# Kernel optimization log

Hardware: AMD Instinct MI355X
Metric: run time of the kernel (lower is better)

The kernel has to match this reference:

```python
import jax, jax.numpy as jnp
import numpy as np

HEADS = 8

def setup_inputs() -> dict:
    key = jax.random.key(0)
    ks = jax.random.split(key, 7)
    B, N, M, C = 4, 2048, 2048, 512
    s = 0.02
    return {
        "hidden_states": jax.random.normal(ks[0], (B, N, C), jnp.float32),
        "encoder_states": jax.random.normal(ks[1], (B, M, C), jnp.float32),
        "Wq": jax.random.normal(ks[2], (C, C), jnp.float32) * s,
        "Wk": jax.random.normal(ks[3], (C, C), jnp.float32) * s,
        "Wv": jax.random.normal(ks[4], (C, C), jnp.float32) * s,
        "Wo": jax.random.normal(ks[5], (C, C), jnp.float32) * s,
        "bo": jnp.zeros((C,), jnp.float32),
    }

def reference(hidden_states, encoder_states, Wq, Wk, Wv, Wo, bo):
    B, N, C = hidden_states.shape
    M = encoder_states.shape[1]
    H = HEADS
    dh = C // H
    scale = dh ** -0.5  # q.shape[-1] ** -0.5 in FlashAttentionFunction / attn.scale
    # projections (to_q/to_k/to_v, no bias as in diffusers CrossAttention)
    q = (hidden_states @ Wq).reshape(B, N, H, dh).transpose(0, 2, 1, 3)   # [B,H,N,dh]
    k = (encoder_states @ Wk).reshape(B, M, H, dh).transpose(0, 2, 1, 3)  # [B,H,M,dh]
    v = (encoder_states @ Wv).reshape(B, M, H, dh).transpose(0, 2, 1, 3)  # [B,H,M,dh]
    # baddbmm(scores) -> softmax -> bmm(values); no mask, non-causal
    scores = jnp.einsum('bhnd,bhmd->bhnm', q, k) * scale                  # [B,H,N,M]
    probs = jax.nn.softmax(scores, axis=-1)
    out = jnp.einsum('bhnm,bhmd->bhnd', probs, v)                         # [B,H,N,dh]
    out = out.transpose(0, 2, 1, 3).reshape(B, N, C)                      # batch_to_head_dim
    return out @ Wo + bo                                                  # to_out[0]; to_out[1] is dropout (identity at eval)
```

## Files before the change

kernel.cpp:

```cpp
#include <hip/hip_runtime.h>
#include <stdint.h>
#include <stddef.h>

typedef __bf16 bf16x8 __attribute__((ext_vector_type(8)));
typedef float f32x4 __attribute__((ext_vector_type(4)));
typedef float f32x16 __attribute__((ext_vector_type(16)));
typedef int int4v __attribute__((ext_vector_type(4)));
typedef unsigned short u16;
typedef unsigned int u32;

__device__ __forceinline__ u16 f2bf(float f) {
    union { float f; unsigned u; } x; x.f = f;
    unsigned r = x.u + 0x7fffu + ((x.u >> 16) & 1u);
    return (u16)(r >> 16);
}

__device__ __forceinline__ float fexp2(float x) { return __builtin_amdgcn_exp2f(x); }

__device__ __forceinline__ u32 cvtpk(float lo, float hi) {
    u32 r;
    asm("v_cvt_pk_bf16_f32 %0, %1, %2" : "=v"(r) : "v"(lo), "v"(hi));
    return r;
}

__device__ __forceinline__ void perm32swap(u32& a, u32& b) {
    asm("v_permlane32_swap_b32 %0, %1" : "+v"(a), "+v"(b));
}

__device__ __forceinline__ f32x16 mfma32(bf16x8 a, bf16x8 b, f32x16 c) {
    return __builtin_amdgcn_mfma_f32_32x32x16_bf16(a, b, c, 0, 0, 0);
}

__device__ __forceinline__ void gl16(const void* g, void* l) {
    __builtin_amdgcn_global_load_lds(
        (const __attribute__((address_space(1))) void*)g,
        (__attribute__((address_space(3))) void*)l, 16, 0, 0);
}

__global__ __launch_bounds__(256) void wtrans4(
        const float* __restrict__ Wq, const float* __restrict__ Wk,
        const float* __restrict__ Wv, const float* __restrict__ Wo,
        u16* __restrict__ oq, u16* __restrict__ ok,
        u16* __restrict__ ov, u16* __restrict__ oo) {
    const int z = blockIdx.z;
    const float* W = (z == 0) ? Wq : (z == 1) ? Wk : (z == 2) ? Wv : Wo;
    u16* O = (z == 0) ? oq : (z == 1) ? ok : (z == 2) ? ov : oo;
    int t  = blockIdx.x * 256 + threadIdx.x;
    int g  = t >> 12;
    int k0 = (t >> 9) & 7;
    int n  = t & 511;
    float v[8];
#pragma unroll
    for (int j = 0; j < 8; ++j)
        v[j] = W[(size_t)(k0 * 64 + g * 8 + j) * 512 + n];
    int gs = g ^ (n & 7);
    u16* dst = O + ((size_t)(k0 * 512 + n) * 8 + gs) * 8;
    ushort4 a, b;
    a.x = f2bf(v[0]); a.y = f2bf(v[1]); a.z = f2bf(v[2]); a.w = f2bf(v[3]);
    b.x = f2bf(v[4]); b.y = f2bf(v[5]); b.z = f2bf(v[6]); b.w = f2bf(v[7]);
    *(ushort4*)dst = a;
    *(ushort4*)(dst + 4) = b;
}

__global__ __launch_bounds__(256) void gemm_qkv(
        const float* __restrict__ hidden, const float* __restrict__ enc,
        const u16* __restrict__ wq, const u16* __restrict__ wk, const u16* __restrict__ wv,
        u16* __restrict__ qo, u16* __restrict__ ko, u16* __restrict__ vo) {
    __shared__ __align__(16) u16 As[128 * 64];
    __shared__ __align__(16) u16 Bs[128 * 64];
    const int z = blockIdx.z;
    const float* A = (z == 0) ? hidden : enc;
    const u16* Bp = (z == 0) ? wq : (z == 1) ? wk : wv;
    const int tid = threadIdx.x, lane = tid & 63, wave = tid >> 6;
    const int wr = (wave >> 1) * 64, wc = (wave & 1) * 64;
    const int brow = blockIdx.x * 128, bcol = blockIdx.y * 128;
    const int lrow = lane & 15;
    const int sr = tid >> 3, sc = tid & 7;

    f32x4 acc[4][4] = {};

    for (int k0s = 0; k0s < 8; ++k0s) {
        const u16* bsrc = Bp + ((size_t)(k0s * 512 + bcol) * 64) + (size_t)(wave * 256 + lane) * 8;
#pragma unroll
        for (int i = 0; i < 4; ++i)
            gl16(bsrc + i * 512, (char*)Bs + wave * 4096 + i * 1024);
#pragma unroll
        for (int i = 0; i < 4; ++i) {
            int r = i * 32 + sr;
            const float* src = A + (size_t)(brow + r) * 512 + k0s * 64 + sc * 8;
            float4 f0 = *(const float4*)src, f1 = *(const float4*)(src + 4);
            int4v w;
            w[0] = cvtpk(f0.x, f0.y); w[1] = cvtpk(f0.z, f0.w);
            w[2] = cvtpk(f1.x, f1.y); w[3] = cvtpk(f1.z, f1.w);
            *(int4v*)((char*)As + r * 128 + ((sc ^ (r & 7)) << 4)) = w;
        }
        __syncthreads();
#pragma unroll
        for (int kc = 0; kc < 2; ++kc) {
            const int kg = kc * 4 + (lane >> 4);
            bf16x8 af[4], bfr[4];
#pragma unroll
            for (int m = 0; m < 4; ++m) {
                int r = wr + m * 16 + lrow;
                af[m] = *(const bf16x8*)((char*)As + r * 128 + ((kg ^ (r & 7)) << 4));
            }
#pragma unroll
            for (int n = 0; n < 4; ++n) {
                int r = wc + n * 16 + lrow;
                bfr[n] = *(const bf16x8*)((char*)Bs + r * 128 + ((kg ^ (r & 7)) << 4));
            }
#pragma unroll
            for (int m = 0; m < 4; ++m)
#pragma unroll
                for (int n = 0; n < 4; ++n)
                    acc[m][n] = __builtin_amdgcn_mfma_f32_16x16x32_bf16(af[m], bfr[n], acc[m][n], 0, 0, 0);
        }
        __syncthreads();
    }

#pragma unroll
    for (int m = 0; m < 4; ++m) {
        int gr0 = brow + wr + m * 16 + ((lane >> 4) << 2);
#pragma unroll
        for (int n = 0; n < 4; ++n) {
            int gc = bcol + wc + n * 16 + lrow;
            int hh = gc >> 6, d = gc & 63;
            int b = gr0 >> 11;
            int bh2 = b * 8 + hh;
            if (z == 0) {
                int nn = gr0 & 2047;
#pragma unroll
                for (int j = 0; j < 4; ++j)
                    qo[((size_t)bh2 * 2048 + nn + j) * 64 + d] =
                        f2bf(acc[m][n][j] * (0.125f * 1.44269504f));
            } else if (z == 1) {
                int kc2 = d >> 4, hl2 = (d >> 3) & 1, e = d & 7;
#pragma unroll
                for (int j = 0; j < 4; ++j) {
                    int nn = (gr0 & 2047) + j;
                    size_t off = (((size_t)bh2 * 64 + (nn >> 5)) * 4 + kc2) * 512
                               + (size_t)((nn & 31) + 32 * hl2) * 8 + e;
                    ko[off] = f2bf(acc[m][n][j]);
                }
            } else {
                int nn0 = gr0 & 2047;
                int slice = ((nn0 >> 4) & 1) * 2 + (d >> 5);
                int lanev = (d & 31) + 32 * ((nn0 >> 3) & 1);
                size_t off = (((size_t)bh2 * 64 + (nn0 >> 5)) * 4 + slice) * 512
                           + (size_t)lanev * 8 + (nn0 & 7);
                ushort4 pk;
                pk.x = f2bf(acc[m][n][0]); pk.y = f2bf(acc[m][n][1]);
                pk.z = f2bf(acc[m][n][2]); pk.w = f2bf(acc[m][n][3]);
                *(ushort4*)(vo + off) = pk;
            }
        }
    }
}

__global__ __launch_bounds__(256) void gemm_out(
        const u16* __restrict__ A, const u16* __restrict__ Bp,
        const float* __restrict__ bias, float* __restrict__ out) {
    __shared__ __align__(16) u16 As[128 * 64];
    __shared__ __align__(16) u16 Bs[64 * 64];
    const int tid = threadIdx.x, lane = tid & 63, wave = tid >> 6;
    const int wr = (wave >> 1) * 64, wc = (wave & 1) * 32;
    const int brow = blockIdx.x * 128, bcol = blockIdx.y * 64;
    const int lrow = lane & 15;
    const int ar = wave * 32 + (lane >> 3), ag = lane & 7;

    f32x4 acc[4][2] = {};

    for (int k0s = 0; k0s < 8; ++k0s) {
        const u16* asrc = A + (size_t)(brow + ar) * 512 + k0s * 64 + ag * 8;
#pragma unroll
        for (int i = 0; i < 4; ++i)
            gl16(asrc + (size_t)(i * 8) * 512, (char*)As + wave * 4096 + i * 1024);
        const u16* bsrc = Bp + ((size_t)(k0s * 512 + bcol) * 64) + (size_t)(wave * 128 + lane) * 8;
#pragma unroll
        for (int i = 0; i < 2; ++i)
            gl16(bsrc + i * 512, (char*)Bs + wave * 2048 + i * 1024);
        __syncthreads();
#pragma unroll
        for (int kc = 0; kc < 2; ++kc) {
            const int kg = kc * 4 + (lane >> 4);
            bf16x8 af[4], bfr[2];
#pragma unroll
            for (int m = 0; m < 4; ++m) {
                int r = wr + m * 16 + lrow;
                af[m] = *(const bf16x8*)((char*)As + r * 128 + ((kg ^ (r & 7)) << 4));
            }
#pragma unroll
            for (int n = 0; n < 2; ++n) {
                int r = wc + n * 16 + lrow;
                bfr[n] = *(const bf16x8*)((char*)Bs + r * 128 + ((kg ^ (r & 7)) << 4));
            }
#pragma unroll
            for (int m = 0; m < 4; ++m)
#pragma unroll
                for (int n = 0; n < 2; ++n)
                    acc[m][n] = __builtin_amdgcn_mfma_f32_16x16x32_bf16(af[m], bfr[n], acc[m][n], 0, 0, 0);
        }
        __syncthreads();
    }

#pragma unroll
    for (int m = 0; m < 4; ++m) {
        int gr0 = brow + wr + m * 16 + ((lane >> 4) << 2);
#pragma unroll
        for (int n = 0; n < 2; ++n) {
            int gc = bcol + wc + n * 16 + lrow;
            float bv = bias[gc];
#pragma unroll
            for (int j = 0; j < 4; ++j)
                out[(size_t)(gr0 + j) * 512 + gc] = acc[m][n][j] + bv;
        }
    }
}

__global__ __launch_bounds__(256, 2) void flash_attn(
        const u16* __restrict__ KQ, const u16* __restrict__ KP,
        const u16* __restrict__ VP, u16* __restrict__ Oa) {
    __shared__ __align__(16) char smem[33280];

    const int tid  = threadIdx.x;
    const int lane = tid & 63;
    const int wave = tid >> 6;
    const int qg   = wave >> 1;
    const int half = wave & 1;
    const int ql   = lane & 31;
    const int hl   = lane >> 5;
    const int bid  = blockIdx.x;
    const int lid  = (bid & 7) * 64 + (bid >> 3);
    const int bh   = lid >> 4;
    const int qt   = lid & 15;
    const int qbase = qt * 128 + qg * 64;

    bf16x8 qf[2][4];
#pragma unroll
    for (int sq = 0; sq < 2; ++sq)
#pragma unroll
        for (int kc = 0; kc < 4; ++kc)
            qf[sq][kc] = *(const bf16x8*)(KQ + ((size_t)bh * 2048 + qbase + sq * 32 + ql) * 64 + kc * 16 + hl * 8);

    const u16* Pb = (qg == 0 ? KP : VP) + ((size_t)bh * 64 + half * 32) * 2048 + lane * 8;
    char* dst0 = smem + half * 8192 + (qg == 0 ? 0 : 4096);

#define STAGE(b_, t_) do { \
    const u16* s_ = Pb + (size_t)(t_) * 2048; \
    char* d_ = dst0 + (b_) * 16384; \
    gl16(s_,        d_); \
    gl16(s_ + 512,  d_ + 1024); \
    gl16(s_ + 1024, d_ + 2048); \
    gl16(s_ + 1536, d_ + 3072); \
} while (0)

    f32x16 acc00 = {}, acc01 = {}, acc10 = {}, acc11 = {};
    float ls[2][4] = {};

    STAGE(0, 0);
    __syncthreads();

    for (int t = 0; t < 32; ++t) {
        const int b = t & 1;
        if (t < 31) STAGE(b ^ 1, t + 1);

        const u16* Kt = (const u16*)(smem + b * 16384 + half * 8192);
        const u16* Vt = Kt + 2048;
        bf16x8 kf[4], vf[2][2];
#pragma unroll
        for (int kc = 0; kc < 4; ++kc)
            kf[kc] = *(const bf16x8*)(Kt + kc * 512 + lane * 8);
#pragma unroll
        for (int jl = 0; jl < 2; ++jl)
#pragma unroll
            for (int dh2 = 0; dh2 < 2; ++dh2)
                vf[jl][dh2] = *(const bf16x8*)(Vt + (jl * 2 + dh2) * 512 + lane * 8);

        f32x16 st0 = {}, st1 = {};
        __builtin_amdgcn_s_setprio(1);
#pragma unroll
        for (int kc = 0; kc < 4; ++kc) {
            st0 = mfma32(kf[kc], qf[0][kc], st0);
            st1 = mfma32(kf[kc], qf[1][kc], st1);
        }
        __builtin_amdgcn_s_setprio(0);

#pragma unroll
        for (int r = 0; r < 16; r += 4) {
            st0[r]   = fexp2(st0[r]);   ls[0][0] += st0[r];
            st0[r+1] = fexp2(st0[r+1]); ls[0][1] += st0[r+1];
            st0[r+2] = fexp2(st0[r+2]); ls[0][2] += st0[r+2];
            st0[r+3] = fexp2(st0[r+3]); ls[0][3] += st0[r+3];
            st1[r]   = fexp2(st1[r]);   ls[1][0] += st1[r];
            st1[r+1] = fexp2(st1[r+1]); ls[1][1] += st1[r+1];
            st1[r+2] = fexp2(st1[r+2]); ls[1][2] += st1[r+2];
            st1[r+3] = fexp2(st1[r+3]); ls[1][3] += st1[r+3];
        }

        __builtin_amdgcn_s_setprio(1);
#pragma unroll
        for (int jl = 0; jl < 2; ++jl) {
            u32 A0 = cvtpk(st0[8*jl+0], st0[8*jl+1]);
            u32 A1 = cvtpk(st0[8*jl+2], st0[8*jl+3]);
            u32 B0 = cvtpk(st0[8*jl+4], st0[8*jl+5]);
            u32 B1 = cvtpk(st0[8*jl+6], st0[8*jl+7]);
            perm32swap(A0, B0);
            perm32swap(A1, B1);
            union { bf16x8 v; u32 u[4]; } bb0;
            bb0.u[0] = A0; bb0.u[1] = A1; bb0.u[2] = B0; bb0.u[3] = B1;
            acc00 = mfma32(vf[jl][0], bb0.v, acc00);
            acc01 = mfma32(vf[jl][1], bb0.v, acc01);
            u32 C0 = cvtpk(st1[8*jl+0], st1[8*jl+1]);
            u32 C1 = cvtpk(st1[8*jl+2], st1[8*jl+3]);
            u32 D0 = cvtpk(st1[8*jl+4], st1[8*jl+5]);
            u32 D1 = cvtpk(st1[8*jl+6], st1[8*jl+7]);
            perm32swap(C0, D0);
            perm32swap(C1, D1);
            union { bf16x8 v; u32 u[4]; } bb1;
            bb1.u[0] = C0; bb1.u[1] = C1; bb1.u[2] = D0; bb1.u[3] = D1;
            acc10 = mfma32(vf[jl][0], bb1.v, acc10);
            acc11 = mfma32(vf[jl][1], bb1.v, acc11);
        }
        __builtin_amdgcn_s_setprio(0);

        __syncthreads();
    }
#undef STAGE

    float lsum0 = (ls[0][0] + ls[0][1]) + (ls[0][2] + ls[0][3]);
    float lsum1 = (ls[1][0] + ls[1][1]) + (ls[1][2] + ls[1][3]);
    lsum0 += __shfl_xor(lsum0, 32);
    lsum1 += __shfl_xor(lsum1, 32);

    float* CB = (float*)smem;
    float* LS = (float*)(smem + 32768);

#define PUBQ(sq, A0, A1, LSV) do { \
    int qq = (sq) * 32 + ql; \
    float* R = CB + qg * 4096 + qq * 64; \
    _Pragma("unroll") \
    for (int rg = 0; rg < 4; ++rg) { \
        int g0 = (2 * rg + hl) ^ (qq & 15); \
        *(f32x4*)(R + g0 * 4) = f32x4{A0[4*rg], A0[4*rg+1], A0[4*rg+2], A0[4*rg+3]}; \
        int g1 = (8 + 2 * rg + hl) ^ (qq & 15); \
        *(f32x4*)(R + g1 * 4) = f32x4{A1[4*rg], A1[4*rg+1], A1[4*rg+2], A1[4*rg+3]}; \
    } \
    if (hl == 0) LS[qg * 64 + qq] = LSV; \
} while (0)

#define REDQ(sq, A0, A1, LSV) do { \
    int qq = (sq) * 32 + ql; \
    const float* R = CB + qg * 4096 + qq * 64; \
    _Pragma("unroll") \
    for (int rg = 0; rg < 4; ++rg) { \
        int g0 = (2 * rg + hl) ^ (qq & 15); \
        f32x4 v0 = *(const f32x4*)(R + g0 * 4); \
        A0[4*rg] += v0[0]; A0[4*rg+1] += v0[1]; A0[4*rg+2] += v0[2]; A0[4*rg+3] += v0[3]; \
        int g1 = (8 + 2 * rg + hl) ^ (qq & 15); \
        f32x4 v1 = *(const f32x4*)(R + g1 * 4); \
        A1[4*rg] += v1[0]; A1[4*rg+1] += v1[1]; A1[4*rg+2] += v1[2]; A1[4*rg+3] += v1[3]; \
    } \
    LSV += LS[qg * 64 + qq]; \
} while (0)

    if (half == 1) {
        PUBQ(0, acc00, acc01, lsum0);
        PUBQ(1, acc10, acc11, lsum1);
    }
    __syncthreads();
    if (half == 0) {
        REDQ(0, acc00, acc01, lsum0);
        REDQ(1, acc10, acc11, lsum1);
        float inv0 = 1.0f / lsum0, inv1 = 1.0f / lsum1;
        int b_ = bh >> 3, hd = bh & 7;
#define STOQ(sq, A0, A1, INV) do { \
        int qrow = qbase + (sq) * 32 + ql; \
        u16* orow = Oa + ((size_t)b_ * 2048 + qrow) * 512 + hd * 64; \
        _Pragma("unroll") \
        for (int rg = 0; rg < 4; ++rg) { \
            int d00 = ((rg ^ (qrow & 7)) << 3) + hl * 4; \
            ushort4 p0; \
            p0.x = f2bf(A0[4*rg] * INV);   p0.y = f2bf(A0[4*rg+1] * INV); \
            p0.z = f2bf(A0[4*rg+2] * INV); p0.w = f2bf(A0[4*rg+3] * INV); \
            *(ushort4*)(orow + d00) = p0; \
            int d01 = (((4 + rg) ^ (qrow & 7)) << 3) + hl * 4; \
            ushort4 p1; \
            p1.x = f2bf(A1[4*rg] * INV);   p1.y = f2bf(A1[4*rg+1] * INV); \
            p1.z = f2bf(A1[4*rg+2] * INV); p1.w = f2bf(A1[4*rg+3] * INV); \
            *(ushort4*)(orow + d01) = p1; \
        } \
} while (0)
        STOQ(0, acc00, acc01, inv0);
        STOQ(1, acc10, acc11, inv1);
#undef STOQ
    }
#undef PUBQ
#undef REDQ
}

extern "C" void kernel_launch(void* const* d_in, const int* in_sizes, int n_in,
                              void* d_out, int out_size, void* d_ws, size_t ws_size,
                              hipStream_t stream) {
    const float* hidden = (const float*)d_in[0];
    const float* enc    = (const float*)d_in[1];
    const float* Wq     = (const float*)d_in[2];
    const float* Wk     = (const float*)d_in[3];
    const float* Wv     = (const float*)d_in[4];
    const float* Wo     = (const float*)d_in[5];
    const float* bo     = (const float*)d_in[6];
    float* out = (float*)d_out;

    char* ws = (char*)d_ws;
    const size_t MB = 1ull << 20;
    u16* q_bf  = (u16*)(ws + 0 * MB);
    u16* kp_bf = (u16*)(ws + 8 * MB);
    u16* vp_bf = (u16*)(ws + 16 * MB);
    u16* at_bf = (u16*)(ws + 24 * MB);
    u16* wq_t  = (u16*)(ws + 32 * MB);
    u16* wk_t  = (u16*)(ws + 32 * MB + 512 * 1024);
    u16* wv_t  = (u16*)(ws + 33 * MB);
    u16* wo_t  = (u16*)(ws + 33 * MB + 512 * 1024);

    dim3 wg(128, 1, 4);
    wtrans4<<<wg, 256, 0, stream>>>(Wq, Wk, Wv, Wo, wq_t, wk_t, wv_t, wo_t);

    dim3 qkvg(64, 4, 3);
    gemm_qkv<<<qkvg, 256, 0, stream>>>(hidden, enc, wq_t, wk_t, wv_t, q_bf, kp_bf, vp_bf);

    flash_attn<<<512, 256, 0, stream>>>(q_bf, kp_bf, vp_bf, at_bf);

    dim3 og(64, 8);
    gemm_out<<<og, 256, 0, stream>>>(at_bf, wo_t, bo, out);
}
```

Before: 87.03 us.

## Halve query tile per flash-attention block and double grid size

Each flash_attn block now handles 64 query rows instead of 128, with each wave-pair covering 32 queries instead of 64, and the grid grows from 512 to 1024 blocks. This lowers register pressure and spreads work across more blocks, so more of the 256 CUs stay busy. In exchange, every K/V tile streamed into shared memory is reused by half as many queries, which doubles global K/V traffic and the per-block staging overhead.

```diff
diff --git a/kernel.cpp b/kernel.cpp
--- a/kernel.cpp
+++ b/kernel.cpp
@@ -218,7 +218,7 @@
 }
 
 __global__ __launch_bounds__(256, 2) void flash_attn(
-        const u16* __restrict__ KQ, const u16* __restrict__ KP,
+        const u16* __restrict__ Q, const u16* __restrict__ KP,
         const u16* __restrict__ VP, u16* __restrict__ Oa) {
     __shared__ __align__(16) char smem[33280];
 
@@ -230,17 +230,15 @@
     const int ql   = lane & 31;
     const int hl   = lane >> 5;
     const int bid  = blockIdx.x;
-    const int lid  = (bid & 7) * 64 + (bid >> 3);
-    const int bh   = lid >> 4;
-    const int qt   = lid & 15;
-    const int qbase = qt * 128 + qg * 64;
-
-    bf16x8 qf[2][4];
-#pragma unroll
-    for (int sq = 0; sq < 2; ++sq)
-#pragma unroll
-        for (int kc = 0; kc < 4; ++kc)
-            qf[sq][kc] = *(const bf16x8*)(KQ + ((size_t)bh * 2048 + qbase + sq * 32 + ql) * 64 + kc * 16 + hl * 8);
+    const int lid  = (bid & 7) * 128 + (bid >> 3);
+    const int bh   = lid >> 5;
+    const int qt   = lid & 31;
+    const int qbase = qt * 64 + qg * 32;
+
+    bf16x8 qf[4];
+#pragma unroll
+    for (int kc = 0; kc < 4; ++kc)
+        qf[kc] = *(const bf16x8*)(Q + ((size_t)bh * 2048 + qbase + ql) * 64 + kc * 16 + hl * 8);
 
     const u16* Pb = (qg == 0 ? KP : VP) + ((size_t)bh * 64 + half * 32) * 2048 + lane * 8;
     char* dst0 = smem + half * 8192 + (qg == 0 ? 0 : 4096);
@@ -254,8 +252,8 @@
     gl16(s_ + 1536, d_ + 3072); \
 } while (0)
 
-    f32x16 acc00 = {}, acc01 = {}, acc10 = {}, acc11 = {};
-    float ls[2][4] = {};
+    f32x16 acc0 = {}, acc1 = {};
+    float ls0 = 0.f, ls1 = 0.f, ls2 = 0.f, ls3 = 0.f;
 
     STAGE(0, 0);
     __syncthreads();
@@ -276,50 +274,34 @@
             for (int dh2 = 0; dh2 < 2; ++dh2)
                 vf[jl][dh2] = *(const bf16x8*)(Vt + (jl * 2 + dh2) * 512 + lane * 8);
 
-        f32x16 st0 = {}, st1 = {};
+        f32x16 st = {};
         __builtin_amdgcn_s_setprio(1);
 #pragma unroll
-        for (int kc = 0; kc < 4; ++kc) {
-            st0 = mfma32(kf[kc], qf[0][kc], st0);
-            st1 = mfma32(kf[kc], qf[1][kc], st1);
-        }
+        for (int kc = 0; kc < 4; ++kc)
+            st = mfma32(kf[kc], qf[kc], st);
         __builtin_amdgcn_s_setprio(0);
 
 #pragma unroll
         for (int r = 0; r < 16; r += 4) {
-            st0[r]   = fexp2(st0[r]);   ls[0][0] += st0[r];
-            st0[r+1] = fexp2(st0[r+1]); ls[0][1] += st0[r+1];
-            st0[r+2] = fexp2(st0[r+2]); ls[0][2] += st0[r+2];
-            st0[r+3] = fexp2(st0[r+3]); ls[0][3] += st0[r+3];
-            st1[r]   = fexp2(st1[r]);   ls[1][0] += st1[r];
-            st1[r+1] = fexp2(st1[r+1]); ls[1][1] += st1[r+1];
-            st1[r+2] = fexp2(st1[r+2]); ls[1][2] += st1[r+2];
-            st1[r+3] = fexp2(st1[r+3]); ls[1][3] += st1[r+3];
+            st[r]   = fexp2(st[r]);   ls0 += st[r];
+            st[r+1] = fexp2(st[r+1]); ls1 += st[r+1];
+            st[r+2] = fexp2(st[r+2]); ls2 += st[r+2];
+            st[r+3] = fexp2(st[r+3]); ls3 += st[r+3];
         }
 
         __builtin_amdgcn_s_setprio(1);
 #pragma unroll
         for (int jl = 0; jl < 2; ++jl) {
-            u32 A0 = cvtpk(st0[8*jl+0], st0[8*jl+1]);
-            u32 A1 = cvtpk(st0[8*jl+2], st0[8*jl+3]);
-            u32 B0 = cvtpk(st0[8*jl+4], st0[8*jl+5]);
-            u32 B1 = cvtpk(st0[8*jl+6], st0[8*jl+7]);
+            u32 A0 = cvtpk(st[8*jl+0], st[8*jl+1]);
+            u32 A1 = cvtpk(st[8*jl+2], st[8*jl+3]);
+            u32 B0 = cvtpk(st[8*jl+4], st[8*jl+5]);
+            u32 B1 = cvtpk(st[8*jl+6], st[8*jl+7]);
             perm32swap(A0, B0);
             perm32swap(A1, B1);
-            union { bf16x8 v; u32 u[4]; } bb0;
-            bb0.u[0] = A0; bb0.u[1] = A1; bb0.u[2] = B0; bb0.u[3] = B1;
-            acc00 = mfma32(vf[jl][0], bb0.v, acc00);
-            acc01 = mfma32(vf[jl][1], bb0.v, acc01);
-            u32 C0 = cvtpk(st1[8*jl+0], st1[8*jl+1]);
-            u32 C1 = cvtpk(st1[8*jl+2], st1[8*jl+3]);
-            u32 D0 = cvtpk(st1[8*jl+4], st1[8*jl+5]);
-            u32 D1 = cvtpk(st1[8*jl+6], st1[8*jl+7]);
-            perm32swap(C0, D0);
-            perm32swap(C1, D1);
-            union { bf16x8 v; u32 u[4]; } bb1;
-            bb1.u[0] = C0; bb1.u[1] = C1; bb1.u[2] = D0; bb1.u[3] = D1;
-            acc10 = mfma32(vf[jl][0], bb1.v, acc10);
-            acc11 = mfma32(vf[jl][1], bb1.v, acc11);
+            union { bf16x8 v; u32 u[4]; } bb;
+            bb.u[0] = A0; bb.u[1] = A1; bb.u[2] = B0; bb.u[3] = B1;
+            acc0 = mfma32(vf[jl][0], bb.v, acc0);
+            acc1 = mfma32(vf[jl][1], bb.v, acc1);
         }
         __builtin_amdgcn_s_setprio(0);
 
@@ -327,72 +309,61 @@
     }
 #undef STAGE
 
-    float lsum0 = (ls[0][0] + ls[0][1]) + (ls[0][2] + ls[0][3]);
-    float lsum1 = (ls[1][0] + ls[1][1]) + (ls[1][2] + ls[1][3]);
-    lsum0 += __shfl_xor(lsum0, 32);
-    lsum1 += __shfl_xor(lsum1, 32);
+    float lsum = (ls0 + ls1) + (ls2 + ls3);
+    lsum += __shfl_xor(lsum, 32);
 
     float* CB = (float*)smem;
-    float* LS = (float*)(smem + 32768);
-
-#define PUBQ(sq, A0, A1, LSV) do { \
-    int qq = (sq) * 32 + ql; \
-    float* R = CB + qg * 4096 + qq * 64; \
+    float* LS = (float*)(smem + 16384);
+
+#define PUBQ(A0, A1, LSV) do { \
+    float* R = CB + qg * 2048 + ql * 64; \
     _Pragma("unroll") \
     for (int rg = 0; rg < 4; ++rg) { \
-        int g0 = (2 * rg + hl) ^ (qq & 15); \
+        int g0 = (2 * rg + hl) ^ (ql & 15); \
         *(f32x4*)(R + g0 * 4) = f32x4{A0[4*rg], A0[4*rg+1], A0[4*rg+2], A0[4*rg+3]}; \
-        int g1 = (8 + 2 * rg + hl) ^ (qq & 15); \
+        int g1 = (8 + 2 * rg + hl) ^ (ql & 15); \
         *(f32x4*)(R + g1 * 4) = f32x4{A1[4*rg], A1[4*rg+1], A1[4*rg+2], A1[4*rg+3]}; \
     } \
-    if (hl == 0) LS[qg * 64 + qq] = LSV; \
+    if (hl == 0) LS[qg * 32 + ql] = LSV; \
 } while (0)
 
-#define REDQ(sq, A0, A1, LSV) do { \
-    int qq = (sq) * 32 + ql; \
-    const float* R = CB + qg * 4096 + qq * 64; \
+#define REDQ(A0, A1, LSV) do { \
+    const float* R = CB + qg * 2048 + ql * 64; \
     _Pragma("unroll") \
     for (int rg = 0; rg < 4; ++rg) { \
-        int g0 = (2 * rg + hl) ^ (qq & 15); \
+        int g0 = (2 * rg + hl) ^ (ql & 15); \
         f32x4 v0 = *(const f32x4*)(R + g0 * 4); \
         A0[4*rg] += v0[0]; A0[4*rg+1] += v0[1]; A0[4*rg+2] += v0[2]; A0[4*rg+3] += v0[3]; \
-        int g1 = (8 + 2 * rg + hl) ^ (qq & 15); \
+        int g1 = (8 + 2 * rg + hl) ^ (ql & 15); \
         f32x4 v1 = *(const f32x4*)(R + g1 * 4); \
         A1[4*rg] += v1[0]; A1[4*rg+1] += v1[1]; A1[4*rg+2] += v1[2]; A1[4*rg+3] += v1[3]; \
     } \
-    LSV += LS[qg * 64 + qq]; \
+    LSV += LS[qg * 32 + ql]; \
 } while (0)
 
     if (half == 1) {
-        PUBQ(0, acc00, acc01, lsum0);
-        PUBQ(1, acc10, acc11, lsum1);
+        PUBQ(acc0, acc1, lsum);
     }
     __syncthreads();
     if (half == 0) {
-        REDQ(0, acc00, acc01, lsum0);
-        REDQ(1, acc10, acc11, lsum1);
-        float inv0 = 1.0f / lsum0, inv1 = 1.0f / lsum1;
+        REDQ(acc0, acc1, lsum);
+        float inv = 1.0f / lsum;
         int b_ = bh >> 3, hd = bh & 7;
-#define STOQ(sq, A0, A1, INV) do { \
-        int qrow = qbase + (sq) * 32 + ql; \
-        u16* orow = Oa + ((size_t)b_ * 2048 + qrow) * 512 + hd * 64; \
-        _Pragma("unroll") \
-        for (int rg = 0; rg < 4; ++rg) { \
-            int d00 = ((rg ^ (qrow & 7)) << 3) + hl * 4; \
-            ushort4 p0; \
-            p0.x = f2bf(A0[4*rg] * INV);   p0.y = f2bf(A0[4*rg+1] * INV); \
-            p0.z = f2bf(A0[4*rg+2] * INV); p0.w = f2bf(A0[4*rg+3] * INV); \
-            *(ushort4*)(orow + d00) = p0; \
-            int d01 = (((4 + rg) ^ (qrow & 7)) << 3) + hl * 4; \
-            ushort4 p1; \
-            p1.x = f2bf(A1[4*rg] * INV);   p1.y = f2bf(A1[4*rg+1] * INV); \
-            p1.z = f2bf(A1[4*rg+2] * INV); p1.w = f2bf(A1[4*rg+3] * INV); \
-            *(ushort4*)(orow + d01) = p1; \
-        } \
-} while (0)
-        STOQ(0, acc00, acc01, inv0);
-        STOQ(1, acc10, acc11, inv1);
-#undef STOQ
+        int qrow = qbase + ql;
+        u16* orow = Oa + ((size_t)b_ * 2048 + qrow) * 512 + hd * 64;
+#pragma unroll
+        for (int rg = 0; rg < 4; ++rg) {
+            int d00 = ((rg ^ (qrow & 7)) << 3) + hl * 4;
+            ushort4 p0;
+            p0.x = f2bf(acc0[4*rg] * inv);   p0.y = f2bf(acc0[4*rg+1] * inv);
+            p0.z = f2bf(acc0[4*rg+2] * inv); p0.w = f2bf(acc0[4*rg+3] * inv);
+            *(ushort4*)(orow + d00) = p0;
+            int d01 = (((4 + rg) ^ (qrow & 7)) << 3) + hl * 4;
+            ushort4 p1;
+            p1.x = f2bf(acc1[4*rg] * inv);   p1.y = f2bf(acc1[4*rg+1] * inv);
+            p1.z = f2bf(acc1[4*rg+2] * inv); p1.w = f2bf(acc1[4*rg+3] * inv);
+            *(ushort4*)(orow + d01) = p1;
+        }
     }
 #undef PUBQ
 #undef REDQ
@@ -427,7 +398,7 @@
     dim3 qkvg(64, 4, 3);
     gemm_qkv<<<qkvg, 256, 0, stream>>>(hidden, enc, wq_t, wk_t, wv_t, q_bf, kp_bf, vp_bf);
 
-    flash_attn<<<512, 256, 0, stream>>>(q_bf, kp_bf, vp_bf, at_bf);
+    flash_attn<<<1024, 256, 0, stream>>>(q_bf, kp_bf, vp_bf, at_bf);
 
     dim3 og(64, 8);
     gemm_out<<<og, 256, 0, stream>>>(at_bf, wo_t, bo, out);
```

Measured after the change: 91.64 us. 1.05x slower.

## Split attention KV across four waves with direct register loads, drop LDS staging

Applied to the files above, without the earlier changes.

The flash attention kernel now gives each block 64 queries, and all four waves share them while each wave handles a quarter of the key/value sequence. The grid doubles to 1024 blocks. K and V tiles are loaded straight from global memory into registers with one-step software prefetch, replacing the double-buffered LDS staging and the per-iteration barrier. Partial accumulators are then reduced serially through a smaller shared buffer over three publish/reduce rounds. This removes synchronization and LDS traffic, at the cost of more global load latency exposure, a longer cross-wave reduction, and Q being loaded redundantly by every wave.

```diff
diff --git a/kernel.cpp b/kernel.cpp
--- a/kernel.cpp
+++ b/kernel.cpp
@@ -217,64 +217,45 @@
     }
 }
 
-__global__ __launch_bounds__(256, 2) void flash_attn(
-        const u16* __restrict__ KQ, const u16* __restrict__ KP,
+__global__ __launch_bounds__(256) void flash_attn(
+        const u16* __restrict__ Q, const u16* __restrict__ KP,
         const u16* __restrict__ VP, u16* __restrict__ Oa) {
-    __shared__ __align__(16) char smem[33280];
+    __shared__ __align__(16) char smem[16640];
 
     const int tid  = threadIdx.x;
     const int lane = tid & 63;
-    const int wave = tid >> 6;
-    const int qg   = wave >> 1;
-    const int half = wave & 1;
+    const int qtr  = tid >> 6;
     const int ql   = lane & 31;
     const int hl   = lane >> 5;
     const int bid  = blockIdx.x;
-    const int lid  = (bid & 7) * 64 + (bid >> 3);
-    const int bh   = lid >> 4;
-    const int qt   = lid & 15;
-    const int qbase = qt * 128 + qg * 64;
+    const int lid  = (bid & 7) * 128 + (bid >> 3);
+    const int bh   = lid >> 5;
+    const int qt   = lid & 31;
+    const int qbase = qt * 64;
 
     bf16x8 qf[2][4];
 #pragma unroll
     for (int sq = 0; sq < 2; ++sq)
 #pragma unroll
         for (int kc = 0; kc < 4; ++kc)
-            qf[sq][kc] = *(const bf16x8*)(KQ + ((size_t)bh * 2048 + qbase + sq * 32 + ql) * 64 + kc * 16 + hl * 8);
-
-    const u16* Pb = (qg == 0 ? KP : VP) + ((size_t)bh * 64 + half * 32) * 2048 + lane * 8;
-    char* dst0 = smem + half * 8192 + (qg == 0 ? 0 : 4096);
-
-#define STAGE(b_, t_) do { \
-    const u16* s_ = Pb + (size_t)(t_) * 2048; \
-    char* d_ = dst0 + (b_) * 16384; \
-    gl16(s_,        d_); \
-    gl16(s_ + 512,  d_ + 1024); \
-    gl16(s_ + 1024, d_ + 2048); \
-    gl16(s_ + 1536, d_ + 3072); \
-} while (0)
+            qf[sq][kc] = *(const bf16x8*)(Q + ((size_t)bh * 2048 + qbase + sq * 32 + ql) * 64 + kc * 16 + hl * 8);
+
+    const u16* Kb = KP + ((size_t)bh * 64 + qtr * 16) * 2048 + lane * 8;
+    const u16* Vb = VP + ((size_t)bh * 64 + qtr * 16) * 2048 + lane * 8;
 
     f32x16 acc00 = {}, acc01 = {}, acc10 = {}, acc11 = {};
     float ls[2][4] = {};
 
-    STAGE(0, 0);
-    __syncthreads();
-
-    for (int t = 0; t < 32; ++t) {
-        const int b = t & 1;
-        if (t < 31) STAGE(b ^ 1, t + 1);
-
-        const u16* Kt = (const u16*)(smem + b * 16384 + half * 8192);
-        const u16* Vt = Kt + 2048;
-        bf16x8 kf[4], vf[2][2];
-#pragma unroll
-        for (int kc = 0; kc < 4; ++kc)
-            kf[kc] = *(const bf16x8*)(Kt + kc * 512 + lane * 8);
-#pragma unroll
-        for (int jl = 0; jl < 2; ++jl)
-#pragma unroll
-            for (int dh2 = 0; dh2 < 2; ++dh2)
-                vf[jl][dh2] = *(const bf16x8*)(Vt + (jl * 2 + dh2) * 512 + lane * 8);
+    bf16x8 kf[4], vf[4];
+#pragma unroll
+    for (int kc = 0; kc < 4; ++kc)
+        kf[kc] = *(const bf16x8*)(Kb + kc * 512);
+#pragma unroll
+    for (int s = 0; s < 4; ++s)
+        vf[s] = *(const bf16x8*)(Vb + s * 512);
+
+    for (int t = 0; t < 16; ++t) {
+        const size_t nxt = (size_t)((t + 1) & 15) * 2048;
 
         f32x16 st0 = {}, st1 = {};
         __builtin_amdgcn_s_setprio(1);
@@ -284,6 +265,10 @@
             st1 = mfma32(kf[kc], qf[1][kc], st1);
         }
         __builtin_amdgcn_s_setprio(0);
+
+#pragma unroll
+        for (int kc = 0; kc < 4; ++kc)
+            kf[kc] = *(const bf16x8*)(Kb + nxt + kc * 512);
 
 #pragma unroll
         for (int r = 0; r < 16; r += 4) {
@@ -308,8 +293,8 @@
             perm32swap(A1, B1);
             union { bf16x8 v; u32 u[4]; } bb0;
             bb0.u[0] = A0; bb0.u[1] = A1; bb0.u[2] = B0; bb0.u[3] = B1;
-            acc00 = mfma32(vf[jl][0], bb0.v, acc00);
-            acc01 = mfma32(vf[jl][1], bb0.v, acc01);
+            acc00 = mfma32(vf[jl*2+0], bb0.v, acc00);
+            acc01 = mfma32(vf[jl*2+1], bb0.v, acc01);
             u32 C0 = cvtpk(st1[8*jl+0], st1[8*jl+1]);
             u32 C1 = cvtpk(st1[8*jl+2], st1[8*jl+3]);
             u32 D0 = cvtpk(st1[8*jl+4], st1[8*jl+5]);
@@ -318,14 +303,15 @@
             perm32swap(C1, D1);
             union { bf16x8 v; u32 u[4]; } bb1;
             bb1.u[0] = C0; bb1.u[1] = C1; bb1.u[2] = D0; bb1.u[3] = D1;
-            acc10 = mfma32(vf[jl][0], bb1.v, acc10);
-            acc11 = mfma32(vf[jl][1], bb1.v, acc11);
+            acc10 = mfma32(vf[jl*2+0], bb1.v, acc10);
+            acc11 = mfma32(vf[jl*2+1], bb1.v, acc11);
         }
         __builtin_amdgcn_s_setprio(0);
 
-        __syncthreads();
-    }
-#undef STAGE
+#pragma unroll
+        for (int s = 0; s < 4; ++s)
+            vf[s] = *(const bf16x8*)(Vb + nxt + s * 512);
+    }
 
     float lsum0 = (ls[0][0] + ls[0][1]) + (ls[0][2] + ls[0][3]);
     float lsum1 = (ls[1][0] + ls[1][1]) + (ls[1][2] + ls[1][3]);
@@ -333,11 +319,11 @@
     lsum1 += __shfl_xor(lsum1, 32);
 
     float* CB = (float*)smem;
-    float* LS = (float*)(smem + 32768);
+    float* LS = (float*)(smem + 16384);
 
 #define PUBQ(sq, A0, A1, LSV) do { \
     int qq = (sq) * 32 + ql; \
-    float* R = CB + qg * 4096 + qq * 64; \
+    float* R = CB + qq * 64; \
     _Pragma("unroll") \
     for (int rg = 0; rg < 4; ++rg) { \
         int g0 = (2 * rg + hl) ^ (qq & 15); \
@@ -345,12 +331,12 @@
         int g1 = (8 + 2 * rg + hl) ^ (qq & 15); \
         *(f32x4*)(R + g1 * 4) = f32x4{A1[4*rg], A1[4*rg+1], A1[4*rg+2], A1[4*rg+3]}; \
     } \
-    if (hl == 0) LS[qg * 64 + qq] = LSV; \
+    if (hl == 0) LS[qq] = LSV; \
 } while (0)
 
 #define REDQ(sq, A0, A1, LSV) do { \
     int qq = (sq) * 32 + ql; \
-    const float* R = CB + qg * 4096 + qq * 64; \
+    const float* R = CB + qq * 64; \
     _Pragma("unroll") \
     for (int rg = 0; rg < 4; ++rg) { \
         int g0 = (2 * rg + hl) ^ (qq & 15); \
@@ -360,17 +346,23 @@
         f32x4 v1 = *(const f32x4*)(R + g1 * 4); \
         A1[4*rg] += v1[0]; A1[4*rg+1] += v1[1]; A1[4*rg+2] += v1[2]; A1[4*rg+3] += v1[3]; \
     } \
-    LSV += LS[qg * 64 + qq]; \
+    LSV += LS[qq]; \
 } while (0)
 
-    if (half == 1) {
-        PUBQ(0, acc00, acc01, lsum0);
-        PUBQ(1, acc10, acc11, lsum1);
-    }
-    __syncthreads();
-    if (half == 0) {
-        REDQ(0, acc00, acc01, lsum0);
-        REDQ(1, acc10, acc11, lsum1);
+    for (int p = 1; p < 4; ++p) {
+        if (qtr == p) {
+            PUBQ(0, acc00, acc01, lsum0);
+            PUBQ(1, acc10, acc11, lsum1);
+        }
+        __syncthreads();
+        if (qtr == 0) {
+            REDQ(0, acc00, acc01, lsum0);
+            REDQ(1, acc10, acc11, lsum1);
+        }
+        __syncthreads();
+    }
+
+    if (qtr == 0) {
         float inv0 = 1.0f / lsum0, inv1 = 1.0f / lsum1;
         int b_ = bh >> 3, hd = bh & 7;
 #define STOQ(sq, A0, A1, INV) do { \
@@ -427,7 +419,7 @@
     dim3 qkvg(64, 4, 3);
     gemm_qkv<<<qkvg, 256, 0, stream>>>(hidden, enc, wq_t, wk_t, wv_t, q_bf, kp_bf, vp_bf);
 
-    flash_attn<<<512, 256, 0, stream>>>(q_bf, kp_bf, vp_bf, at_bf);
+    flash_attn<<<1024, 256, 0, stream>>>(q_bf, kp_bf, vp_bf, at_bf);
 
     dim3 og(64, 8);
     gemm_out<<<og, 256, 0, stream>>>(at_bf, wo_t, bo, out);
```

Result: slower. 98.66 us (+13.4%).

## Split flash-attention blocks into 2-wave groups with per-wave private K/V staging

Applied to the files above, without the earlier changes.

Blocks are halved to two waves covering a 64-row query tile, and the grid doubles to 1024 blocks. Each wave now loads its own K and V halves into a private double buffer and waits with explicit vmcnt counts, so the per-iteration block-wide __syncthreads goes away. The K/V staging that used to be shared between the two query groups is no longer shared, so each K/V tile is fetched twice as often from global/L2. A single barrier before the cross-wave reduction is kept.

```diff
diff --git a/kernel.cpp b/kernel.cpp
--- a/kernel.cpp
+++ b/kernel.cpp
@@ -217,54 +217,62 @@
     }
 }
 
-__global__ __launch_bounds__(256, 2) void flash_attn(
-        const u16* __restrict__ KQ, const u16* __restrict__ KP,
+__global__ __launch_bounds__(128) void flash_attn(
+        const u16* __restrict__ Q, const u16* __restrict__ KP,
         const u16* __restrict__ VP, u16* __restrict__ Oa) {
-    __shared__ __align__(16) char smem[33280];
+    __shared__ __align__(16) char smem[32768];
 
     const int tid  = threadIdx.x;
     const int lane = tid & 63;
-    const int wave = tid >> 6;
-    const int qg   = wave >> 1;
-    const int half = wave & 1;
+    const int half = tid >> 6;
     const int ql   = lane & 31;
     const int hl   = lane >> 5;
     const int bid  = blockIdx.x;
-    const int lid  = (bid & 7) * 64 + (bid >> 3);
-    const int bh   = lid >> 4;
-    const int qt   = lid & 15;
-    const int qbase = qt * 128 + qg * 64;
+    const int lid  = (bid & 7) * 128 + (bid >> 3);
+    const int bh   = lid >> 5;
+    const int qt   = lid & 31;
+    const int qbase = qt * 64;
 
     bf16x8 qf[2][4];
 #pragma unroll
     for (int sq = 0; sq < 2; ++sq)
 #pragma unroll
         for (int kc = 0; kc < 4; ++kc)
-            qf[sq][kc] = *(const bf16x8*)(KQ + ((size_t)bh * 2048 + qbase + sq * 32 + ql) * 64 + kc * 16 + hl * 8);
-
-    const u16* Pb = (qg == 0 ? KP : VP) + ((size_t)bh * 64 + half * 32) * 2048 + lane * 8;
-    char* dst0 = smem + half * 8192 + (qg == 0 ? 0 : 4096);
+            qf[sq][kc] = *(const bf16x8*)(Q + ((size_t)bh * 2048 + qbase + sq * 32 + ql) * 64 + kc * 16 + hl * 8);
+
+    const u16* Kb = KP + ((size_t)bh * 64 + half * 32) * 2048 + lane * 8;
+    const u16* Vb = VP + ((size_t)bh * 64 + half * 32) * 2048 + lane * 8;
+    char* my = smem + half * 16384;
 
 #define STAGE(b_, t_) do { \
-    const u16* s_ = Pb + (size_t)(t_) * 2048; \
-    char* d_ = dst0 + (b_) * 16384; \
-    gl16(s_,        d_); \
-    gl16(s_ + 512,  d_ + 1024); \
-    gl16(s_ + 1024, d_ + 2048); \
-    gl16(s_ + 1536, d_ + 3072); \
+    const u16* ks_ = Kb + (size_t)(t_) * 2048; \
+    const u16* vs_ = Vb + (size_t)(t_) * 2048; \
+    char* d_ = my + (b_) * 8192; \
+    gl16(ks_,        d_); \
+    gl16(ks_ + 512,  d_ + 1024); \
+    gl16(ks_ + 1024, d_ + 2048); \
+    gl16(ks_ + 1536, d_ + 3072); \
+    gl16(vs_,        d_ + 4096); \
+    gl16(vs_ + 512,  d_ + 5120); \
+    gl16(vs_ + 1024, d_ + 6144); \
+    gl16(vs_ + 1536, d_ + 7168); \
 } while (0)
 
     f32x16 acc00 = {}, acc01 = {}, acc10 = {}, acc11 = {};
     float ls[2][4] = {};
 
     STAGE(0, 0);
-    __syncthreads();
-
+    int buf = 0;
     for (int t = 0; t < 32; ++t) {
-        const int b = t & 1;
-        if (t < 31) STAGE(b ^ 1, t + 1);
-
-        const u16* Kt = (const u16*)(smem + b * 16384 + half * 8192);
+        if (t < 31) {
+            STAGE(buf ^ 1, t + 1);
+            asm volatile("s_waitcnt vmcnt(8)" ::: "memory");
+        } else {
+            asm volatile("s_waitcnt vmcnt(0)" ::: "memory");
+        }
+        __builtin_amdgcn_sched_barrier(0);
+
+        const u16* Kt = (const u16*)(my + buf * 8192);
         const u16* Vt = Kt + 2048;
         bf16x8 kf[4], vf[2][2];
 #pragma unroll
@@ -323,7 +331,7 @@
         }
         __builtin_amdgcn_s_setprio(0);
 
-        __syncthreads();
+        buf ^= 1;
     }
 #undef STAGE
 
@@ -333,11 +341,11 @@
     lsum1 += __shfl_xor(lsum1, 32);
 
     float* CB = (float*)smem;
-    float* LS = (float*)(smem + 32768);
+    float* LS = (float*)(smem + 16384);
 
 #define PUBQ(sq, A0, A1, LSV) do { \
     int qq = (sq) * 32 + ql; \
-    float* R = CB + qg * 4096 + qq * 64; \
+    float* R = CB + qq * 64; \
     _Pragma("unroll") \
     for (int rg = 0; rg < 4; ++rg) { \
         int g0 = (2 * rg + hl) ^ (qq & 15); \
@@ -345,12 +353,12 @@
         int g1 = (8 + 2 * rg + hl) ^ (qq & 15); \
         *(f32x4*)(R + g1 * 4) = f32x4{A1[4*rg], A1[4*rg+1], A1[4*rg+2], A1[4*rg+3]}; \
     } \
-    if (hl == 0) LS[qg * 64 + qq] = LSV; \
+    if (hl == 0) LS[qq] = LSV; \
 } while (0)
 
 #define REDQ(sq, A0, A1, LSV) do { \
     int qq = (sq) * 32 + ql; \
-    const float* R = CB + qg * 4096 + qq * 64; \
+    const float* R = CB + qq * 64; \
     _Pragma("unroll") \
     for (int rg = 0; rg < 4; ++rg) { \
         int g0 = (2 * rg + hl) ^ (qq & 15); \
@@ -360,9 +368,10 @@
         f32x4 v1 = *(const f32x4*)(R + g1 * 4); \
         A1[4*rg] += v1[0]; A1[4*rg+1] += v1[1]; A1[4*rg+2] += v1[2]; A1[4*rg+3] += v1[3]; \
     } \
-    LSV += LS[qg * 64 + qq]; \
+    LSV += LS[qq]; \
 } while (0)
 
+    __syncthreads();
     if (half == 1) {
         PUBQ(0, acc00, acc01, lsum0);
         PUBQ(1, acc10, acc11, lsum1);
@@ -427,7 +436,7 @@
     dim3 qkvg(64, 4, 3);
     gemm_qkv<<<qkvg, 256, 0, stream>>>(hidden, enc, wq_t, wk_t, wv_t, q_bf, kp_bf, vp_bf);
 
-    flash_attn<<<512, 256, 0, stream>>>(q_bf, kp_bf, vp_bf, at_bf);
+    flash_attn<<<1024, 128, 0, stream>>>(q_bf, kp_bf, vp_bf, at_bf);
 
     dim3 og(64, 8);
     gemm_out<<<og, 256, 0, stream>>>(at_bf, wo_t, bo, out);
```

New measurement: 97.69 us. +12.2%, slower.
